# Optimization experiments

Hardware: AMD Instinct MI355X
Metric: run time of the kernel (lower is better)

## Reference

```python
import jax, jax.numpy as jnp
import numpy as np
from math import sqrt

MIN_SCORE = 0.05
MAX_OVERLAP = 0.45
TOP_K = 200


def make_priors():
    feature_dims = {'mid': 18, 'end': 9, 'a': 9, 'b': 5, 'c': 3, 'd': 1}
    obj_scales = {'mid': 0.2, 'end': 0.2, 'a': 0.375, 'b': 0.55, 'c': 0.725, 'd': 0.9}
    aspect_ratio = {'mid': [1.0, 2.0, 3.0, 0.5, 0.333], 'end': [1.0, 2.0, 3.0, 0.5, 0.333],
                    'a': [1.0, 2.0, 3.0, 0.5, 0.333], 'b': [1.0, 2.0, 3.0, 0.5, 0.333],
                    'c': [1.0, 2.0, 0.5], 'd': [1.0, 2.0, 0.5]}
    fmaps = list(feature_dims.keys())
    boxes = []
    for k, fmap in enumerate(fmaps):
        for i in range(feature_dims[fmap]):
            for j in range(feature_dims[fmap]):
                cx = (j + 0.5) / feature_dims[fmap]
                cy = (i + 0.5) / feature_dims[fmap]
                for ratio in aspect_ratio[fmap]:
                    boxes.append([cx, cy, obj_scales[fmap] * sqrt(ratio), obj_scales[fmap] / sqrt(ratio)])
                if fmap in ['mid', 'end', 'a', 'b', 'c']:
                    s = sqrt(obj_scales[fmap] * obj_scales[fmaps[k + 1]])
                else:
                    s = 1.0
                boxes.append([cx, cy, s, s])
    return np.clip(np.asarray(boxes, dtype=np.float32), 0.0, 1.0)  # [3106, 4]


def setup_inputs() -> dict:
    key = jax.random.key(0)
    k1, k2 = jax.random.split(key)
    return {
        'predicted_locs': jax.random.normal(k1, (4, 3106, 4), dtype=jnp.float32),
        'predicted_scores': jax.random.normal(k2, (4, 3106, 21), dtype=jnp.float32),
        'priors_cxcy': jnp.asarray(make_priors()),
    }


def _decode(predicted_locs, priors):
    # gcxgcy_to_cxcy then cxcy_to_xy (standard SSD variances 0.1 / 0.2)
    cxcy = predicted_locs[..., :2] * priors[..., 2:] / 10.0 + priors[..., :2]
    wh = jnp.exp(predicted_locs[..., 2:] / 5.0) * priors[..., 2:]
    return jnp.concatenate([cxcy - wh / 2.0, cxcy + wh / 2.0], axis=-1)  # xyxy


def _detect_image(boxes_i, probs_i):
    # boxes_i: [P,4] xyxy, probs_i: [P,C] softmax scores
    P = boxes_i.shape[0]
    C = probs_i.shape[1]
    # full pairwise Jaccard overlap [P,P]
    lt = jnp.maximum(boxes_i[:, None, :2], boxes_i[None, :, :2])
    rb = jnp.minimum(boxes_i[:, None, 2:], boxes_i[None, :, 2:])
    inter = jnp.prod(jnp.clip(rb - lt, 0.0), axis=-1)
    area = jnp.prod(boxes_i[:, 2:] - boxes_i[:, :2], axis=-1)
    iou = inter / (area[:, None] + area[None, :] - inter)

    cls = probs_i[:, 1:].T                      # [C-1, P], skip background
    valid = cls > MIN_SCORE
    order = jnp.argsort(-jnp.where(valid, cls, -jnp.inf), axis=1)  # [C-1, P]
    valid_s = jnp.take_along_axis(valid, order, axis=1)
    iou_sg = jax.lax.stop_gradient(iou)

    def body(i, suppress):                       # greedy NMS over sorted boxes, all classes at once
        bi = order[:, i]                         # [C-1] prior index per class
        rows = jnp.take_along_axis(iou_sg[bi], order, axis=1) > MAX_OVERLAP  # [C-1, P]
        skip = suppress[:, i] | ~valid_s[:, i]
        proc = (suppress | rows).at[:, i].set(False)
        return jnp.where(skip[:, None], suppress, proc)

    suppress = jax.lax.fori_loop(0, P, body, ~valid_s)
    keep = ~suppress                             # [C-1, P] (sorted order)

    scores_s = jnp.take_along_axis(cls, order, axis=1)
    cand_scores = jnp.where(keep, scores_s, -jnp.inf).reshape(-1)     # [(C-1)*P]
    cand_boxes = boxes_i[order].reshape(-1, 4)
    cand_labels = jnp.broadcast_to(jnp.arange(1, C, dtype=jnp.int32)[:, None], (C - 1, P)).reshape(-1)

    top_scores, top_idx = jax.lax.top_k(cand_scores, TOP_K)
    top_boxes = cand_boxes[top_idx]
    top_labels = cand_labels[top_idx]

    has = jnp.isfinite(top_scores)
    top_scores = jnp.where(has, top_scores, 0.0)
    top_boxes = jnp.where(has[:, None], top_boxes, 0.0)
    top_labels = jnp.where(has, top_labels, 0)
    count = jnp.minimum(jnp.sum(keep).astype(jnp.int32), TOP_K)

    # torch fallback: a single background box when nothing is detected
    none = count == 0
    top_boxes = top_boxes.at[0].set(jnp.where(none, jnp.array([0.0, 0.0, 1.0, 1.0], dtype=top_boxes.dtype), top_boxes[0]))
    count = jnp.where(none, jnp.int32(1), count)
    return top_boxes, top_labels, top_scores, count


def reference(predicted_locs, predicted_scores, priors_cxcy):
    probs = jax.nn.softmax(predicted_scores, axis=2)          # [B,P,C]
    boxes = _decode(predicted_locs, priors_cxcy[None])        # [B,P,4]
    all_boxes, all_labels, all_scores, counts = jax.vmap(_detect_image)(boxes, probs)
    return all_boxes, all_labels, all_scores, counts
```

## Files before the change

kernel.cpp:

```cpp
#include <hip/hip_runtime.h>

#define NB 4
#define NPRI 3106
#define NC 21
#define NCLS 20
#define KMAX 200
#define NMAX 1024
#define WMAX 16
#define TMAX (WMAX*(WMAX+1)/2)
#define MIN_SC 0.05f
#define MAX_OV 0.45f

#define F_PROBS 0
#define F_KEYS  (F_PROBS + NB*NCLS*NPRI)
#define F_BOXES (F_KEYS + NB*NCLS*NMAX*2)
#define F_AREAS (F_BOXES + NB*NCLS*NMAX*4)
#define F_NCAND (F_AREAS + NB*NCLS*NMAX)
#define F_M     (F_NCAND + 128)
#define F_POOL  (F_M + NB*NCLS*WMAX*NMAX*2)
#define F_CNT   (F_POOL + NB*NCLS*KMAX*2)
#define F_DONE  (F_CNT + NB*NCLS)

#define OUT_BOXES  0
#define OUT_LABELS (NB*KMAX*4)
#define OUT_SCORES (OUT_LABELS + NB*KMAX)
#define OUT_COUNTS (OUT_SCORES + NB*KMAX)

__device__ __forceinline__ float bcast(float v, int l) {
    return __uint_as_float(__builtin_amdgcn_readlane(__float_as_uint(v), l));
}

__device__ __forceinline__ void decode_box(const float* __restrict__ locs,
                                           const float* __restrict__ priors,
                                           int b, int pi,
                                           float& x1, float& y1, float& x2, float& y2) {
    const float* l  = locs + ((size_t)b * NPRI + pi) * 4;
    const float* pr = priors + (size_t)pi * 4;
    float pcx = pr[0], pcy = pr[1], pw = pr[2], ph = pr[3];
    float cx = l[0] * pw / 10.0f + pcx;
    float cy = l[1] * ph / 10.0f + pcy;
    float w  = expf(l[2] / 5.0f) * pw;
    float h  = expf(l[3] / 5.0f) * ph;
    x1 = cx - w / 2.0f;  y1 = cy - h / 2.0f;
    x2 = cx + w / 2.0f;  y2 = cy + h / 2.0f;
}

__device__ __forceinline__ unsigned long long shfl_xor_u64(unsigned long long v, int m) {
    unsigned lo = (unsigned)v, hi = (unsigned)(v >> 32);
    lo = __shfl_xor(lo, m);
    hi = __shfl_xor(hi, m);
    return ((unsigned long long)hi << 32) | lo;
}

__global__ __launch_bounds__(1024)
void det_prep(const float* __restrict__ scores, const float* __restrict__ locs,
              const float* __restrict__ priors, float* __restrict__ ws) {
    const int bc  = blockIdx.x;
    const int b   = bc / NCLS;
    const int c   = bc - b * NCLS;
    const int tid = threadIdx.x;

    __shared__ unsigned long long keys[NMAX];
    __shared__ int n_sh;
    if (tid == 0) n_sh = 0;
    __syncthreads();

    const float* sbase = scores + (size_t)b * NPRI * NC;
    for (int r = tid; r < NPRI; r += 1024) {
        const float* s = sbase + (size_t)r * NC;
        float m = -1e30f;
        #pragma unroll
        for (int k = 0; k < NC; ++k) m = fmaxf(m, s[k]);
        float sum = 0.0f, ec = 0.0f;
        #pragma unroll
        for (int k = 0; k < NC; ++k) {
            float e = expf(s[k] - m);
            sum += e;
            if (k == c + 1) ec = e;
        }
        float val = ec / sum;
        if (val > MIN_SC) {
            int idx = atomicAdd(&n_sh, 1);
            if (idx < NMAX) {
                unsigned int sb = __float_as_uint(val);
                keys[idx] = ((unsigned long long)(~sb) << 32)
                          | (unsigned int)r;
            }
        }
    }
    __syncthreads();
    int n = n_sh; if (n > NMAX) n = NMAX;

    unsigned long long mykey = (tid < n) ? keys[tid] : ~0ull;
    __syncthreads();
    for (int k = 2; k <= NMAX; k <<= 1) {
        for (int j = k >> 1; j > 0; j >>= 1) {
            unsigned long long other;
            if (j >= 64) {
                keys[tid] = mykey;
                __syncthreads();
                other = keys[tid ^ j];
                __syncthreads();
            } else {
                other = shfl_xor_u64(mykey, j);
            }
            bool lower    = (tid & j) == 0;
            bool up       = (tid & k) == 0;
            bool take_min = (lower == up);
            bool swap     = take_min ? (other < mykey) : (other > mykey);
            mykey = swap ? other : mykey;
        }
    }

    if (tid == 0) ((int*)(ws + F_NCAND))[bc] = n;
    unsigned long long* gk = (unsigned long long*)(ws + F_KEYS) + (size_t)bc * NMAX;
    float4* gb = (float4*)(ws + F_BOXES) + (size_t)bc * NMAX;
    float*  ga = ws + F_AREAS + (size_t)bc * NMAX;
    if (tid < n) {
        gk[tid] = mykey;
        int pi = (int)(mykey & 0xFFFFFFFFull);
        float x1, y1, x2, y2;
        decode_box(locs, priors, b, pi, x1, y1, x2, y2);
        gb[tid] = make_float4(x1, y1, x2, y2);
        ga[tid] = (x2 - x1) * (y2 - y1);
    }
}

__global__ __launch_bounds__(256)
void det_mbuild(float* __restrict__ ws) {
    if (blockIdx.x == 0 && blockIdx.y == 0 && threadIdx.x < NB)
        ((int*)(ws + F_DONE))[threadIdx.x] = 0;

    const int bc = blockIdx.y;
    const int t  = blockIdx.x * 4 + (threadIdx.x >> 6);
    if (t >= TMAX) return;
    const int lane = threadIdx.x & 63;
    int tj = 0;
    while ((tj + 1) * (tj + 2) / 2 <= t) ++tj;
    const int w = t - tj * (tj + 1) / 2;
    const int n = ((const int*)(ws + F_NCAND))[bc];
    const int bi0 = w * 64, bj0 = tj * 64;
    if (bj0 >= n) return;

    const float4* bx = (const float4*)(ws + F_BOXES) + (size_t)bc * NMAX;
    const float*  ar = ws + F_AREAS + (size_t)bc * NMAX;
    const float4 bi = bx[bi0 + lane];
    const float  ai = ar[bi0 + lane];
    const float4 bj = bx[bj0 + lane];
    const float  aj = ar[bj0 + lane];
    const unsigned long long vm =
        (n - bi0 >= 64) ? ~0ull : ((1ull << (n - bi0)) - 1ull);
    const bool diag = (w == tj);
    unsigned long long myword = 0ull;

    #pragma unroll
    for (int jj = 0; jj < 64; jj += 2) {
        float ax1 = bcast(bj.x, jj),     ay1 = bcast(bj.y, jj);
        float ax2 = bcast(bj.z, jj),     ay2 = bcast(bj.w, jj);
        float aau = bcast(aj, jj);
        float bx1 = bcast(bj.x, jj + 1), by1 = bcast(bj.y, jj + 1);
        float bx2 = bcast(bj.z, jj + 1), by2 = bcast(bj.w, jj + 1);
        float bau = bcast(aj, jj + 1);

        float alx = fmaxf(bi.x, ax1), aly = fmaxf(bi.y, ay1);
        float arx = fminf(bi.z, ax2), ary = fminf(bi.w, ay2);
        float blx = fmaxf(bi.x, bx1), bly = fmaxf(bi.y, by1);
        float brx = fminf(bi.z, bx2), bry = fminf(bi.w, by2);
        float adx = fmaxf(arx - alx, 0.0f), ady = fmaxf(ary - aly, 0.0f);
        float bdx = fmaxf(brx - blx, 0.0f), bdy = fmaxf(bry - bly, 0.0f);
        float ain = adx * ady;
        float bin = bdx * bdy;
        float au  = ai + aau - ain;
        float bu  = ai + bau - bin;
        float at  = MAX_OV * au;
        float bt  = MAX_OV * bu;
        bool akeep = ain > at;
        bool bkeep = bin > bt;
        bool anear = fabsf(ain - at) <= at * 6e-7f;
        bool bnear = fabsf(bin - bt) <= bt * 6e-7f;
        if (__ballot(anear || bnear)) {
            float aio = ain / au;
            float bio = bin / bu;
            akeep = anear ? (aio > MAX_OV) : akeep;
            bkeep = bnear ? (bio > MAX_OV) : bkeep;
        }
        unsigned long long abits = __ballot(akeep) & vm;
        unsigned long long bbits = __ballot(bkeep) & vm;
        if (diag) {
            abits &= (1ull << jj) - 1ull;
            bbits &= (1ull << (jj + 1)) - 1ull;
        }
        if (lane == jj)     myword = abits;
        if (lane == jj + 1) myword = bbits;
    }
    if (bj0 + lane < n)
        ((unsigned long long*)(ws + F_M))
            [((size_t)bc * WMAX + w) * NMAX + bj0 + lane] = myword;
}

__global__ __launch_bounds__(256)
void det_finish(const float* __restrict__ locs, const float* __restrict__ priors,
                float* __restrict__ ws, float* __restrict__ out) {
    const int bc   = blockIdx.x;
    const int b    = bc / NCLS;
    const int c    = bc - b * NCLS;
    const int cls  = c + 1;
    const int tid  = threadIdx.x;
    int* done_i = (int*)(ws + F_DONE);

    if (tid < 64) {
        const int lane = tid;
        const int n    = ((const int*)(ws + F_NCAND))[bc];
        const unsigned long long* Mb =
            (const unsigned long long*)(ws + F_M) + (size_t)bc * WMAX * NMAX;

        unsigned long long kw[WMAX];
        #pragma unroll
        for (int w = 0; w < WMAX; ++w) kw[w] = 0ull;

        const unsigned long long lmask = (1ull << lane) - 1ull;
        #pragma unroll
        for (int w = 0; w < WMAX; ++w) {
            if (w * 64 < n) {
                int cc = w * 64 + lane;
                bool valid = cc < n;
                unsigned long long pre = 0ull;
                #pragma unroll
                for (int v = 0; v < WMAX; ++v)
                    if (v < w) pre |= Mb[(size_t)v * NMAX + cc] & kw[v];
                unsigned long long dg = Mb[(size_t)w * NMAX + cc] & lmask;
                bool sup0 = (pre != 0ull);
                unsigned long long K = __ballot(valid && !sup0);
                for (int it = 0; it < 64; ++it) {
                    bool sup = sup0 || ((dg & K) != 0ull);
                    unsigned long long Kn = __ballot(valid && !sup);
                    if (Kn == K) break;
                    K = Kn;
                }
                kw[w] = K;
            }
        }

        int pref[WMAX + 1];
        pref[0] = 0;
        #pragma unroll
        for (int w = 0; w < WMAX; ++w) pref[w + 1] = pref[w] + __popcll(kw[w]);
        if (lane == 0) ((int*)(ws + F_CNT))[bc] = pref[WMAX];

        const unsigned long long* gk =
            (const unsigned long long*)(ws + F_KEYS) + (size_t)bc * NMAX;
        unsigned long long* pool =
            (unsigned long long*)(ws + F_POOL) + (size_t)bc * KMAX;
        const unsigned long long ctag = (unsigned long long)(cls << 12);
        #pragma unroll
        for (int w = 0; w < WMAX; ++w) {
            unsigned long long kwv = kw[w];
            int cc = w * 64 + lane;
            if (cc < n && ((kwv >> lane) & 1ull)) {
                int pos = pref[w] + __popcll(kwv & lmask);
                if (pos < KMAX) pool[pos] = gk[cc] | ctag;
            }
        }
    }

    {
        int idx = c * 256 + tid;
        if (idx < KMAX * 4) {
            out[OUT_BOXES + (size_t)b * KMAX * 4 + idx] = 0.0f;
        } else if (idx < KMAX * 4 + KMAX) {
            out[OUT_LABELS + b * KMAX + (idx - KMAX * 4)] = 0.0f;
        } else if (idx < KMAX * 4 + 2 * KMAX) {
            out[OUT_SCORES + b * KMAX + (idx - KMAX * 4 - KMAX)] = 0.0f;
        }
    }

    __threadfence();
    __syncthreads();
    if (tid == 0)
        __hip_atomic_fetch_add(done_i + b, 1, __ATOMIC_RELEASE,
                               __HIP_MEMORY_SCOPE_AGENT);

    if (tid == 0) {
        int it = 0;
        while (__hip_atomic_load(done_i + b, __ATOMIC_ACQUIRE,
                                 __HIP_MEMORY_SCOPE_AGENT) < NCLS
               && it < (1 << 20)) ++it;
    }
    __syncthreads();

    __shared__ unsigned long long lpool[NCLS * KMAX];
    __shared__ int cnts[NCLS];

    const int* cnt = (const int*)(ws + F_CNT);
    if (tid < NCLS) cnts[tid] = cnt[b * NCLS + tid];
    __syncthreads();

    const unsigned long long* pool =
        (const unsigned long long*)(ws + F_POOL) + (size_t)b * NCLS * KMAX;
    for (int i = tid; i < NCLS * KMAX; i += 256) {
        int c2 = i / KMAX, r = i - c2 * KMAX;
        int mc2 = cnts[c2] < KMAX ? cnts[c2] : KMAX;
        lpool[i] = (r < mc2) ? pool[i] : ~0ull;
    }
    __syncthreads();

    if (c == 0 && tid == 0) {
        int tot = 0;
        for (int c2 = 0; c2 < NCLS; ++c2) tot += cnts[c2];
        int count = tot < KMAX ? tot : KMAX;
        if (tot == 0) {
            float* ob = out + OUT_BOXES + (size_t)b * KMAX * 4;
            ob[0] = 0.0f; ob[1] = 0.0f; ob[2] = 1.0f; ob[3] = 1.0f;
            count = 1;
        }
        out[OUT_COUNTS + b] = (float)count;
    }

    const int mc = cnts[c] < KMAX ? cnts[c] : KMAX;
    if (tid < mc) {
        unsigned long long key = lpool[c * KMAX + tid];
        int rank = 0;
        #pragma unroll
        for (int c2 = 0; c2 < NCLS; ++c2) {
            int lo = 0, hi = KMAX;
            #pragma unroll
            for (int s = 0; s < 8; ++s) {
                int mid = (lo + hi) >> 1;
                int midc = mid < KMAX ? mid : KMAX - 1;
                unsigned long long v = lpool[c2 * KMAX + midc];
                bool lt = (lo < hi) && (v < key);
                lo = lt ? mid + 1 : lo;
                hi = lt ? hi : mid;
            }
            rank += lo;
        }
        if (rank < KMAX) {
            unsigned int lo32 = (unsigned int)key;
            int pi  = lo32 & 0xFFF;
            int lab = (lo32 >> 12) & 0x1F;
            float sc = __uint_as_float(~(unsigned int)(key >> 32));
            float x1, y1, x2, y2;
            decode_box(locs, priors, b, pi, x1, y1, x2, y2);
            float* ob = out + OUT_BOXES + ((size_t)b * KMAX + rank) * 4;
            ob[0] = x1; ob[1] = y1; ob[2] = x2; ob[3] = y2;
            out[OUT_LABELS + b * KMAX + rank] = (float)lab;
            out[OUT_SCORES + b * KMAX + rank] = sc;
        }
    }
}

extern "C" void kernel_launch(void* const* d_in, const int* in_sizes, int n_in,
                              void* d_out, int out_size, void* d_ws, size_t ws_size,
                              hipStream_t stream) {
    const float* locs   = (const float*)d_in[0];
    const float* scores = (const float*)d_in[1];
    const float* priors = (const float*)d_in[2];
    float* out = (float*)d_out;
    float* ws  = (float*)d_ws;

    det_prep<<<NB * NCLS, 1024, 0, stream>>>(scores, locs, priors, ws);
    det_mbuild<<<dim3((TMAX + 3) / 4, NB * NCLS), 256, 0, stream>>>(ws);
    det_finish<<<NB * NCLS, 256, 0, stream>>>(locs, priors, ws, out);
}
```

Before: 156.4 us.

## Split finish kernel at grid barrier and preload softmax rows per thread

```diff
diff --git a/kernel.cpp b/kernel.cpp
--- a/kernel.cpp
+++ b/kernel.cpp
@@ -52,6 +52,29 @@
     return ((unsigned long long)hi << 32) | lo;
 }
 
+__device__ __forceinline__ void softmax_push(const float* __restrict__ v, int c,
+                                             int r, unsigned long long* keys,
+                                             int* n_sh) {
+    float m = -1e30f;
+    #pragma unroll
+    for (int k = 0; k < NC; ++k) m = fmaxf(m, v[k]);
+    float sum = 0.0f, ec = 0.0f;
+    #pragma unroll
+    for (int k = 0; k < NC; ++k) {
+        float e = expf(v[k] - m);
+        sum += e;
+        if (k == c + 1) ec = e;
+    }
+    float val = ec / sum;
+    if (val > MIN_SC) {
+        int idx = atomicAdd(n_sh, 1);
+        if (idx < NMAX) {
+            unsigned int sb = __float_as_uint(val);
+            keys[idx] = ((unsigned long long)(~sb) << 32) | (unsigned int)r;
+        }
+    }
+}
+
 __global__ __launch_bounds__(1024)
 void det_prep(const float* __restrict__ scores, const float* __restrict__ locs,
               const float* __restrict__ priors, float* __restrict__ ws) {
@@ -66,26 +89,26 @@
     __syncthreads();
 
     const float* sbase = scores + (size_t)b * NPRI * NC;
-    for (int r = tid; r < NPRI; r += 1024) {
-        const float* s = sbase + (size_t)r * NC;
-        float m = -1e30f;
-        #pragma unroll
-        for (int k = 0; k < NC; ++k) m = fmaxf(m, s[k]);
-        float sum = 0.0f, ec = 0.0f;
-        #pragma unroll
-        for (int k = 0; k < NC; ++k) {
-            float e = expf(s[k] - m);
-            sum += e;
-            if (k == c + 1) ec = e;
-        }
-        float val = ec / sum;
-        if (val > MIN_SC) {
-            int idx = atomicAdd(&n_sh, 1);
-            if (idx < NMAX) {
-                unsigned int sb = __float_as_uint(val);
-                keys[idx] = ((unsigned long long)(~sb) << 32)
-                          | (unsigned int)r;
-            }
+    {
+        float v0[NC], v1[NC], v2[NC];
+        const float* s0 = sbase + (size_t)(tid)        * NC;
+        const float* s1 = sbase + (size_t)(tid + 1024) * NC;
+        const float* s2 = sbase + (size_t)(tid + 2048) * NC;
+        #pragma unroll
+        for (int k = 0; k < NC; ++k) { v0[k] = s0[k]; }
+        #pragma unroll
+        for (int k = 0; k < NC; ++k) { v1[k] = s1[k]; }
+        #pragma unroll
+        for (int k = 0; k < NC; ++k) { v2[k] = s2[k]; }
+        softmax_push(v0, c, tid,        keys, &n_sh);
+        softmax_push(v1, c, tid + 1024, keys, &n_sh);
+        softmax_push(v2, c, tid + 2048, keys, &n_sh);
+        if (tid < NPRI - 3072) {
+            float v3[NC];
+            const float* s3 = sbase + (size_t)(tid + 3072) * NC;
+            #pragma unroll
+            for (int k = 0; k < NC; ++k) { v3[k] = s3[k]; }
+            softmax_push(v3, c, tid + 3072, keys, &n_sh);
         }
     }
     __syncthreads();
@@ -199,14 +222,12 @@
 }
 
 __global__ __launch_bounds__(256)
-void det_finish(const float* __restrict__ locs, const float* __restrict__ priors,
-                float* __restrict__ ws, float* __restrict__ out) {
+void det_finishA(float* __restrict__ ws, float* __restrict__ out) {
     const int bc   = blockIdx.x;
     const int b    = bc / NCLS;
     const int c    = bc - b * NCLS;
     const int cls  = c + 1;
     const int tid  = threadIdx.x;
-    int* done_i = (int*)(ws + F_DONE);
 
     if (tid < 64) {
         const int lane = tid;
@@ -273,20 +294,15 @@
             out[OUT_SCORES + b * KMAX + (idx - KMAX * 4 - KMAX)] = 0.0f;
         }
     }
-
-    __threadfence();
-    __syncthreads();
-    if (tid == 0)
-        __hip_atomic_fetch_add(done_i + b, 1, __ATOMIC_RELEASE,
-                               __HIP_MEMORY_SCOPE_AGENT);
-
-    if (tid == 0) {
-        int it = 0;
-        while (__hip_atomic_load(done_i + b, __ATOMIC_ACQUIRE,
-                                 __HIP_MEMORY_SCOPE_AGENT) < NCLS
-               && it < (1 << 20)) ++it;
-    }
-    __syncthreads();
+}
+
+__global__ __launch_bounds__(256)
+void det_finishB(const float* __restrict__ locs, const float* __restrict__ priors,
+                 const float* __restrict__ ws, float* __restrict__ out) {
+    const int bc   = blockIdx.x;
+    const int b    = bc / NCLS;
+    const int c    = bc - b * NCLS;
+    const int tid  = threadIdx.x;
 
     __shared__ unsigned long long lpool[NCLS * KMAX];
     __shared__ int cnts[NCLS];
@@ -360,5 +376,6 @@
 
     det_prep<<<NB * NCLS, 1024, 0, stream>>>(scores, locs, priors, ws);
     det_mbuild<<<dim3((TMAX + 3) / 4, NB * NCLS), 256, 0, stream>>>(ws);
-    det_finish<<<NB * NCLS, 256, 0, stream>>>(locs, priors, ws, out);
-}
+    det_finishA<<<NB * NCLS, 256, 0, stream>>>(ws, out);
+    det_finishB<<<NB * NCLS, 256, 0, stream>>>(locs, priors, ws, out);
+}
```

Measured after the change: 149.4 us. -4.5%, faster.
